# Kernel optimization log

Measured on AMD Instinct MI355X. Metric: run time of the kernel, lower is better.

The kernel has to match this reference:

```python
import jax, jax.numpy as jnp
import numpy as np

ALPHA = 0.2
NEG_INF = -9e15


def setup_inputs() -> dict:
    key = jax.random.key(0)
    k1, k2, k3, k4 = jax.random.split(key, 4)
    B, N, C_IN, C_OUT, R, H = 8, 1024, 256, 256, 4, 4
    node_feats = jax.random.normal(k1, (B, N, C_IN), dtype=jnp.float32)
    adj_matrix = jax.random.randint(k2, (B, N, N, R), 0, 2, dtype=jnp.int32)
    # xavier_uniform with gain=1.414 for Linear(c_in, c_out) weights
    lim_w = 1.414 * np.sqrt(6.0 / (C_IN + C_OUT))
    W = jax.random.uniform(k3, (R, C_IN, C_OUT), minval=-lim_w, maxval=lim_w, dtype=jnp.float32)
    c_per = C_OUT // H
    lim_a = 1.414 * np.sqrt(6.0 / (H + 2 * c_per))
    a = jax.random.uniform(k4, (R, H, 2 * c_per), minval=-lim_a, maxval=lim_a, dtype=jnp.float32)
    return {"node_feats": node_feats, "adj_matrix": adj_matrix, "W": W, "a": a}


def reference(node_feats, adj_matrix, W, a):
    B, N, _ = node_feats.shape
    R, H = a.shape[0], a.shape[1]
    C = a.shape[2] // 2  # per-head feature dim
    out = jnp.zeros((B, N, H, C), dtype=node_feats.dtype)
    for r in range(R):
        # per-relation projection: [B,N,H,C]
        f = jnp.einsum('bnc,cd->bnd', node_feats, W[r]).reshape(B, N, H, C)
        a_l, a_r = a[r, :, :C], a[r, :, C:]
        # attention logit decomposes: a . [f_i || f_j] = a_l . f_i + a_r . f_j
        li = jnp.einsum('bnhc,hc->bnh', f, a_l)  # source-node term
        lj = jnp.einsum('bnhc,hc->bnh', f, a_r)  # target-node term
        logits = jax.nn.leaky_relu(li[:, :, None, :] + lj[:, None, :, :], ALPHA)  # [B,N,N,H]
        mask = adj_matrix[..., r] != 0  # [B,N,N]
        logits = jnp.where(mask[..., None], logits, NEG_INF)
        probs = jax.nn.softmax(logits, axis=2)
        out = out + jnp.einsum('bijh,bjhc->bihc', probs, f)
    # concat_heads=True
    return out.reshape(B, N, H * C)
```

## Files before the change

### kernel.cpp

```cpp
#include <hip/hip_runtime.h>
#include <math.h>

#define Bsz 8
#define Nn 1024
#define CIN 256
#define COUT 256
#define NR 4
#define NH 4

typedef unsigned short u16;
typedef __attribute__((ext_vector_type(8))) short bf16x8;
typedef __attribute__((ext_vector_type(4))) float f32x4;
typedef __attribute__((ext_vector_type(2))) float f32x2;

#define OFF_EEI (16u << 20)
#define OFF_EEJ (17u << 20)
#define OFF_ADJM (18u << 20)
#define OFF_XBF (22u << 20)
#define OFF_WBFT (26u << 20)
#define OFF_WAL ((26u << 20) + (512u << 10))
#define OFF_WAR ((26u << 20) + (528u << 10))

#define LOG2E 1.4426950408889634f

__device__ __forceinline__ short f2bf(float x) {
  union { float f; unsigned u; } v; v.f = x;
  unsigned r = (v.u + 0x7FFFu + ((v.u >> 16) & 1u)) >> 16;
  return (short)r;
}

__device__ __forceinline__ float fast_exp2(float x) {
#if __has_builtin(__builtin_amdgcn_exp2f)
  return __builtin_amdgcn_exp2f(x);
#else
  return exp2f(x);
#endif
}

__device__ __forceinline__ int sbfe1(unsigned v, int bit) {
#if __has_builtin(__builtin_amdgcn_sbfe)
  return __builtin_amdgcn_sbfe((int)v, bit, 1);
#else
  return ((int)(v << (31 - bit))) >> 31;
#endif
}

__device__ __forceinline__ unsigned perm_hi16(unsigned hi, unsigned lo) {
#if __has_builtin(__builtin_amdgcn_perm)
  return __builtin_amdgcn_perm(hi, lo, 0x07060302u);
#else
  return (lo >> 16) | (hi & 0xFFFF0000u);
#endif
}

__device__ __forceinline__ void gl_lds16(const void* g, void* l) {
  __builtin_amdgcn_global_load_lds(
      (const __attribute__((address_space(1))) unsigned int*)(unsigned long long)g,
      (__attribute__((address_space(3))) unsigned int*)(unsigned int)(unsigned long long)l,
      16, 0, 0);
}

__global__ __launch_bounds__(256, 8)
void gatt_pack(const int4* __restrict__ adj4, unsigned long long* __restrict__ adjm) {
  const int t = threadIdx.x;
  const int wid = blockIdx.x * 4 + (t >> 6);
  const int lane = t & 63;
  const int jw = wid & 15;
  const int i = (wid >> 4) & 1023;
  const int b = wid >> 14;
  const int j = jw * 64 + lane;
  const int4 av = adj4[(size_t)(b * Nn + i) * Nn + j];
  const unsigned long long b0 = __ballot(av.x != 0);
  const unsigned long long b1 = __ballot(av.y != 0);
  const unsigned long long b2 = __ballot(av.z != 0);
  const unsigned long long b3 = __ballot(av.w != 0);
  if (lane < 4) {
    unsigned long long v = (lane == 0) ? b0 : (lane == 1) ? b1 : (lane == 2) ? b2 : b3;
    adjm[((size_t)((b * Nn + i) * NR + lane)) * 16 + jw] = v;
  }
}

__global__ __launch_bounds__(256, 4)
void gatt_prep(const float* __restrict__ W, const float* __restrict__ a,
               u16* __restrict__ WbfT, float* __restrict__ wa_l,
               float* __restrict__ wa_r) {
  const int t = threadIdx.x;
  if (blockIdx.x < 32) {
    const int r = blockIdx.x >> 3, kc = blockIdx.x & 7;
    u16 pk[32];
#pragma unroll 8
    for (int kk = 0; kk < 32; ++kk)
      pk[kk] = (u16)f2bf(W[(size_t)r * 65536 + (size_t)(kc * 32 + kk) * COUT + t]);
    u16* dst = WbfT + (size_t)r * 65536 + (size_t)t * CIN + kc * 32;
#pragma unroll
    for (int q = 0; q < 4; ++q) *(int4*)(dst + q * 8) = *(int4*)(pk + q * 8);
  } else {
    const int cb = blockIdx.x - 32;
    const int r = cb >> 2, h = cb & 3;
    float sl = 0.f, sr = 0.f;
    const float* Wp = W + (size_t)r * 65536 + (size_t)t * COUT + h * 64;
    const float* ap = a + r * 512 + h * 128;
#pragma unroll 8
    for (int c = 0; c < 64; ++c) {
      const float wv = Wp[c];
      sl = fmaf(wv, ap[c], sl);
      sr = fmaf(wv, ap[64 + c], sr);
    }
    wa_l[(size_t)cb * CIN + t] = sl;
    wa_r[(size_t)cb * CIN + t] = sr;
  }
}

__global__ __launch_bounds__(256, 4)
void gatt_logitx(const float* __restrict__ X, const float4* __restrict__ wal4,
                 const float4* __restrict__ war4, float2* __restrict__ EEi,
                 float2* __restrict__ EEj, u16* __restrict__ Xbf) {
  __shared__ float Xs[16 * 260];
  const int t = threadIdx.x;
  const int row0 = blockIdx.x * 16;
  {
    const int il = t >> 4, kq = t & 15;
    const float4* xp = (const float4*)(X + (size_t)(row0 + il) * CIN + kq * 16);
    float4 v[4];
    u16 pk[16];
#pragma unroll
    for (int u = 0; u < 4; ++u) {
      v[u] = xp[u];
      pk[u * 4 + 0] = (u16)f2bf(v[u].x);
      pk[u * 4 + 1] = (u16)f2bf(v[u].y);
      pk[u * 4 + 2] = (u16)f2bf(v[u].z);
      pk[u * 4 + 3] = (u16)f2bf(v[u].w);
    }
    float4* dst = (float4*)(Xs + il * 260 + kq * 16);
#pragma unroll
    for (int u = 0; u < 4; ++u) dst[u] = v[u];
    u16* xb = Xbf + (size_t)(row0 + il) * CIN + kq * 16;
    *(int4*)xb = *(int4*)pk;
    *(int4*)(xb + 8) = *(int4*)(pk + 8);
  }
  __syncthreads();
  const int rl = t >> 4, combo = t & 15;
  float li = 0.f, lj = 0.f;
#pragma unroll 8
  for (int k4 = 0; k4 < 64; ++k4) {
    const float4 x4 = *(const float4*)(Xs + rl * 260 + k4 * 4);
    const float4 wl = wal4[combo * 64 + k4];
    const float4 wr = war4[combo * 64 + k4];
    li += x4.x * wl.x + x4.y * wl.y + x4.z * wl.z + x4.w * wl.w;
    lj += x4.x * wr.x + x4.y * wr.y + x4.z * wr.z + x4.w * wr.w;
  }
  const int g = row0 + rl, b = g >> 10, n = g & 1023;
  const size_t idx = ((size_t)(combo * Bsz + b)) * Nn + n;
  const float lis = li * LOG2E, ljs = lj * LOG2E;
  EEi[idx] = make_float2(fast_exp2(lis), fast_exp2(0.2f * lis));
  EEj[idx] = make_float2(fast_exp2(ljs), fast_exp2(0.2f * ljs));
}

__global__ __launch_bounds__(256)
void gatt_fgemm(const u16* __restrict__ Xbf, const u16* __restrict__ WbfT,
                u16* __restrict__ fTf) {
  __shared__ u16 lds_w[8192];
  __shared__ u16 lds_x[2048];
  const int t = threadIdx.x;
  const int r = blockIdx.x & 3, b = (blockIdx.x >> 2) & 7, ntl = blockIdx.x >> 5;
  const int n0 = ntl * 64;
  const int g0 = b * Nn + n0;
  const int lane = t & 63, w = t >> 6;
  const int m = lane & 15, quad = lane >> 4;
  const int cw = w * 64;
  const int xq = quad ^ (m & 3);

  const u16* Wsrc = WbfT + (size_t)r * 65536;
  f32x4 acc[4][4];
#pragma unroll
  for (int ct = 0; ct < 4; ++ct)
#pragma unroll
    for (int nt = 0; nt < 4; ++nt) acc[ct][nt] = (f32x4){0.f, 0.f, 0.f, 0.f};

  for (int kc = 0; kc < 8; ++kc) {
    __syncthreads();
#pragma unroll
    for (int q = 0; q < 4; ++q) {
      const int s = q * 256 + t;
      const int c = s >> 2, ks = (s & 3) ^ (c & 3);
      gl_lds16(Wsrc + (size_t)c * CIN + kc * 32 + ks * 8, lds_w + s * 8);
    }
    {
      const int s = t;
      const int n = s >> 2, ks = (s & 3) ^ (n & 3);
      gl_lds16(Xbf + (size_t)(g0 + n) * CIN + kc * 32 + ks * 8, lds_x + s * 8);
    }
    __syncthreads();

    bf16x8 af[4], bfr[4];
#pragma unroll
    for (int ct = 0; ct < 4; ++ct)
      af[ct] = *(const bf16x8*)(lds_w + (cw + ct * 16 + m) * 32 + xq * 8);
#pragma unroll
    for (int nt = 0; nt < 4; ++nt)
      bfr[nt] = *(const bf16x8*)(lds_x + (nt * 16 + m) * 32 + xq * 8);
#pragma unroll
    for (int ct = 0; ct < 4; ++ct)
#pragma unroll
      for (int nt = 0; nt < 4; ++nt)
        acc[ct][nt] = __builtin_amdgcn_mfma_f32_16x16x32_bf16(af[ct], bfr[nt], acc[ct][nt], 0, 0, 0);
  }

  u16* fragbase = fTf + (size_t)(((r * Bsz + b) * 4 + w) * 128) * 512;
#pragma unroll
  for (int ct = 0; ct < 4; ++ct) {
#pragma unroll
    for (int ntf = 0; ntf < 4; ++ntf) {
      const int j = n0 + ntf * 16 + m;
      const int jb = j >> 5;
      const int qt = ((ntf & 1) << 1) | (m >> 3);
      const int e = m & 7;
      u16* dst = fragbase + (size_t)((jb * 4 + ct) * 512) + (qt * 16 + quad * 4) * 8 + e;
#pragma unroll
      for (int p = 0; p < 4; ++p) dst[p * 8] = (u16)f2bf(acc[ct][ntf][p]);
    }
  }
}

__global__ __launch_bounds__(1024, 4)
void gatt_attn(const unsigned long long* __restrict__ adjm,
               const u16* __restrict__ fTf, const float2* __restrict__ EEi,
               const float2* __restrict__ EEj, float* __restrict__ out) {
  __shared__ float smem[16384];

  const int t = threadIdx.x;
  const int b = blockIdx.x & 7;
  const int i0 = (blockIdx.x >> 3) * 32;
  const int w = t >> 6, lane = t & 63;
  const int r = w & 3, h = w >> 2;
  const int m = lane & 15, quad = lane >> 4;
  const int qo = quad * 8;
  const int combo = r * NH + h;

  const float2* EEib = EEi + ((size_t)(combo * Bsz + b)) * Nn;
  const float2 Li0 = EEib[i0 + m];
  const float2 Li1 = EEib[i0 + 16 + m];
  const f32x2 EI0 = {Li0.x, Li0.y};
  const f32x2 EI1 = {Li1.x, Li1.y};
  const float4* ej4 = (const float4*)(smem + combo * 1024);

  const unsigned long long* amp0 = adjm + ((size_t)((b * Nn + i0 + m) * NR + r)) * 16;
  const unsigned long long* amp1 = adjm + ((size_t)((b * Nn + i0 + 16 + m) * NR + r)) * 16;
  const bf16x8* fp = (const bf16x8*)fTf + (size_t)(((r * Bsz + b) * 4 + h)) * 8192;

  bf16x8 ones;
#pragma unroll
  for (int e = 0; e < 8; ++e) ones[e] = (short)0x3F80;

  f32x4 acc[2][4], den[2];
#pragma unroll
  for (int iw = 0; iw < 2; ++iw) {
    den[iw] = (f32x4){0.f, 0.f, 0.f, 0.f};
#pragma unroll
    for (int nt = 0; nt < 4; ++nt) acc[iw][nt] = (f32x4){0.f, 0.f, 0.f, 0.f};
  }

  for (int hs = 0; hs < 2; ++hs) {
    {
#pragma unroll
      for (int q = 0; q < 4; ++q) {
        const int s = q * 1024 + t;
        const int cb = s >> 8, off = s & 255;
        ((float4*)smem)[s] =
            ((const float4*)(EEj + ((size_t)(cb * Bsz + b)) * Nn))[hs * 256 + off];
      }
    }
    __syncthreads();

    for (int jq = hs * 8; jq < hs * 8 + 8; ++jq) {
      const uint2 mw0 = *(const uint2*)(amp0 + jq);
      const uint2 mw1 = *(const uint2*)(amp1 + jq);
#pragma unroll
      for (int half = 0; half < 2; ++half) {
        const int jb = jq * 2 + half;
        const int jbl = jb & 15;
        const unsigned mb0 = (half ? mw0.y : mw0.x) >> qo;
        const unsigned mb1 = (half ? mw1.y : mw1.x) >> qo;
        bf16x8 bfr[4];
#pragma unroll
        for (int nt = 0; nt < 4; ++nt) bfr[nt] = fp[(jb * 4 + nt) * 64 + lane];
        unsigned afu0[4], afu1[4];
#pragma unroll
        for (int pr = 0; pr < 4; ++pr) {
          const float4 v = ej4[jbl * 16 + quad * 4 + pr];
          const f32x2 v01 = {v.x, v.y};
          const f32x2 v23 = {v.z, v.w};
          {
            const f32x2 a0 = v01 * EI0;
            const f32x2 a1 = v23 * EI0;
            const unsigned e0 =
                __float_as_uint(fmaxf(a0.x, a0.y)) & (unsigned)sbfe1(mb0, 2 * pr);
            const unsigned e1 =
                __float_as_uint(fmaxf(a1.x, a1.y)) & (unsigned)sbfe1(mb0, 2 * pr + 1);
            afu0[pr] = perm_hi16(e1, e0);
          }
          {
            const f32x2 a0 = v01 * EI1;
            const f32x2 a1 = v23 * EI1;
            const unsigned e0 =
                __float_as_uint(fmaxf(a0.x, a0.y)) & (unsigned)sbfe1(mb1, 2 * pr);
            const unsigned e1 =
                __float_as_uint(fmaxf(a1.x, a1.y)) & (unsigned)sbfe1(mb1, 2 * pr + 1);
            afu1[pr] = perm_hi16(e1, e0);
          }
        }
        union { unsigned u[4]; bf16x8 v; } af0, af1;
#pragma unroll
        for (int pr = 0; pr < 4; ++pr) { af0.u[pr] = afu0[pr]; af1.u[pr] = afu1[pr]; }
        den[0] = __builtin_amdgcn_mfma_f32_16x16x32_bf16(af0.v, ones, den[0], 0, 0, 0);
#pragma unroll
        for (int nt = 0; nt < 4; ++nt)
          acc[0][nt] = __builtin_amdgcn_mfma_f32_16x16x32_bf16(af0.v, bfr[nt], acc[0][nt], 0, 0, 0);
        den[1] = __builtin_amdgcn_mfma_f32_16x16x32_bf16(af1.v, ones, den[1], 0, 0, 0);
#pragma unroll
        for (int nt = 0; nt < 4; ++nt)
          acc[1][nt] = __builtin_amdgcn_mfma_f32_16x16x32_bf16(af1.v, bfr[nt], acc[1][nt], 0, 0, 0);
      }
    }
    __syncthreads();
  }

#define OSTRIDE 260
#pragma unroll
  for (int rr = 0; rr < 4; ++rr) {
    if (r == rr) {
#pragma unroll
      for (int iw = 0; iw < 2; ++iw) {
#pragma unroll
        for (int p = 0; p < 4; ++p) {
          const float inv = __builtin_amdgcn_rcpf(den[iw][p]);
          float* op = smem + (iw * 16 + quad * 4 + p) * OSTRIDE + h * 64 + m;
#pragma unroll
          for (int nt = 0; nt < 4; ++nt) {
            const float v = acc[iw][nt][p] * inv;
            if (rr == 0) op[nt * 16] = v;
            else op[nt * 16] += v;
          }
        }
      }
    }
    __syncthreads();
  }

#pragma unroll
  for (int q = 0; q < 2; ++q) {
    const int idx = q * 1024 + t;
    const int row = idx >> 6, c4 = idx & 63;
    const float4 v = *(const float4*)(smem + row * OSTRIDE + c4 * 4);
    ((float4*)out)[((size_t)(b * Nn + i0 + row)) * 64 + c4] = v;
  }
}

extern "C" void kernel_launch(void* const* d_in, const int* in_sizes, int n_in,
                              void* d_out, int out_size, void* d_ws, size_t ws_size,
                              hipStream_t stream) {
  const float* X = (const float*)d_in[0];
  const int4* adj4 = (const int4*)d_in[1];
  const float* W = (const float*)d_in[2];
  const float* a = (const float*)d_in[3];
  float* out = (float*)d_out;

  char* ws = (char*)d_ws;
  u16* fTf = (u16*)ws;
  float2* EEi = (float2*)(ws + OFF_EEI);
  float2* EEj = (float2*)(ws + OFF_EEJ);
  unsigned long long* adjm = (unsigned long long*)(ws + OFF_ADJM);
  u16* Xbf = (u16*)(ws + OFF_XBF);
  u16* WbfT = (u16*)(ws + OFF_WBFT);
  float* wa_l = (float*)(ws + OFF_WAL);
  float* wa_r = (float*)(ws + OFF_WAR);

  gatt_pack<<<dim3(32768), dim3(256), 0, stream>>>(adj4, adjm);
  gatt_prep<<<dim3(48), dim3(256), 0, stream>>>(W, a, WbfT, wa_l, wa_r);
  gatt_logitx<<<dim3(512), dim3(256), 0, stream>>>(X, (const float4*)wa_l,
                                                   (const float4*)wa_r, EEi, EEj, Xbf);
  gatt_fgemm<<<dim3(512), dim3(256), 0, stream>>>(Xbf, WbfT, fTf);
  gatt_attn<<<dim3(256), dim3(1024), 0, stream>>>(adjm, fTf, EEi, EEj, out);
}
```

Baseline: 289.1 us.

## Split adjacency packing across prep, logit and GEMM kernels as extra blocks

Removes the standalone adjacency bit-packing kernel and spreads its 32768 blocks over the three preparatory kernels as extra trailing blocks. The bandwidth-bound packing can then run alongside the small, latency-bound prep, logit and projection GEMM work, which removes one launch and fills idle CUs. The risk is that the heavy packing blocks compete with the GEMM for bandwidth and occupancy. The GEMM kernel's launch bounds also limit how many packing blocks fit per CU.

```diff
diff --git a/kernel.cpp b/kernel.cpp
--- a/kernel.cpp
+++ b/kernel.cpp
@@ -23,6 +23,10 @@
 
 #define LOG2E 1.4426950408889634f
 
+#define PK_PREP 3072
+#define PK_LGX 6144
+#define PK_TOTAL 32768
+
 __device__ __forceinline__ short f2bf(float x) {
   union { float f; unsigned u; } v; v.f = x;
   unsigned r = (v.u + 0x7FFFu + ((v.u >> 16) & 1u)) >> 16;
@@ -60,10 +64,9 @@
       16, 0, 0);
 }
 
-__global__ __launch_bounds__(256, 8)
-void gatt_pack(const int4* __restrict__ adj4, unsigned long long* __restrict__ adjm) {
-  const int t = threadIdx.x;
-  const int wid = blockIdx.x * 4 + (t >> 6);
+__device__ __forceinline__ void pack_body(int pbid, int t, const int4* __restrict__ adj4,
+                                          unsigned long long* __restrict__ adjm) {
+  const int wid = pbid * 4 + (t >> 6);
   const int lane = t & 63;
   const int jw = wid & 15;
   const int i = (wid >> 4) & 1023;
@@ -83,8 +86,13 @@
 __global__ __launch_bounds__(256, 4)
 void gatt_prep(const float* __restrict__ W, const float* __restrict__ a,
                u16* __restrict__ WbfT, float* __restrict__ wa_l,
-               float* __restrict__ wa_r) {
+               float* __restrict__ wa_r, const int4* __restrict__ adj4,
+               unsigned long long* __restrict__ adjm) {
   const int t = threadIdx.x;
+  if (blockIdx.x >= 48) {
+    pack_body(blockIdx.x - 48, t, adj4, adjm);
+    return;
+  }
   if (blockIdx.x < 32) {
     const int r = blockIdx.x >> 3, kc = blockIdx.x & 7;
     u16 pk[32];
@@ -114,9 +122,14 @@
 __global__ __launch_bounds__(256, 4)
 void gatt_logitx(const float* __restrict__ X, const float4* __restrict__ wal4,
                  const float4* __restrict__ war4, float2* __restrict__ EEi,
-                 float2* __restrict__ EEj, u16* __restrict__ Xbf) {
+                 float2* __restrict__ EEj, u16* __restrict__ Xbf,
+                 const int4* __restrict__ adj4, unsigned long long* __restrict__ adjm) {
   __shared__ float Xs[16 * 260];
   const int t = threadIdx.x;
+  if (blockIdx.x >= 512) {
+    pack_body(blockIdx.x - 512 + PK_PREP, t, adj4, adjm);
+    return;
+  }
   const int row0 = blockIdx.x * 16;
   {
     const int il = t >> 4, kq = t & 15;
@@ -158,10 +171,15 @@
 
 __global__ __launch_bounds__(256)
 void gatt_fgemm(const u16* __restrict__ Xbf, const u16* __restrict__ WbfT,
-                u16* __restrict__ fTf) {
+                u16* __restrict__ fTf, const int4* __restrict__ adj4,
+                unsigned long long* __restrict__ adjm) {
   __shared__ u16 lds_w[8192];
   __shared__ u16 lds_x[2048];
   const int t = threadIdx.x;
+  if (blockIdx.x >= 512) {
+    pack_body(blockIdx.x - 512 + PK_PREP + PK_LGX, t, adj4, adjm);
+    return;
+  }
   const int r = blockIdx.x & 3, b = (blockIdx.x >> 2) & 7, ntl = blockIdx.x >> 5;
   const int n0 = ntl * 64;
   const int g0 = b * Nn + n0;
@@ -375,10 +393,11 @@
   float* wa_l = (float*)(ws + OFF_WAL);
   float* wa_r = (float*)(ws + OFF_WAR);
 
-  gatt_pack<<<dim3(32768), dim3(256), 0, stream>>>(adj4, adjm);
-  gatt_prep<<<dim3(48), dim3(256), 0, stream>>>(W, a, WbfT, wa_l, wa_r);
-  gatt_logitx<<<dim3(512), dim3(256), 0, stream>>>(X, (const float4*)wa_l,
-                                                   (const float4*)wa_r, EEi, EEj, Xbf);
-  gatt_fgemm<<<dim3(512), dim3(256), 0, stream>>>(Xbf, WbfT, fTf);
+  gatt_prep<<<dim3(48 + PK_PREP), dim3(256), 0, stream>>>(W, a, WbfT, wa_l, wa_r,
+                                                          adj4, adjm);
+  gatt_logitx<<<dim3(512 + PK_LGX), dim3(256), 0, stream>>>(
+      X, (const float4*)wa_l, (const float4*)wa_r, EEi, EEj, Xbf, adj4, adjm);
+  gatt_fgemm<<<dim3(512 + (PK_TOTAL - PK_PREP - PK_LGX)), dim3(256), 0, stream>>>(
+      Xbf, WbfT, fTf, adj4, adjm);
   gatt_attn<<<dim3(256), dim3(1024), 0, stream>>>(adjm, fTf, EEi, EEj, out);
 }
```

After: 283.2 us, median of 2. 1.02x faster.

## Fuse adjacency bit-packing into attention kernel with register-prefetched mask tiles

Applied to the files above, without the earlier changes.

Removes the separate adjacency pack kernel. The attention kernel now reads the int32 adjacency directly, ballots it into bitmasks held in shared memory, and prefetches the next 128-column chunk (adjacency and EEj) into registers while the MFMA work on the current chunk runs. This drops one kernel launch and the write and re-read of the packed mask through global memory. In exchange the attention kernel carries more registers and two barriers per chunk, and its 128 MB adjacency stream now overlaps with compute.

```diff
diff --git a/kernel.cpp b/kernel.cpp
--- a/kernel.cpp
+++ b/kernel.cpp
@@ -15,7 +15,6 @@
 
 #define OFF_EEI (16u << 20)
 #define OFF_EEJ (17u << 20)
-#define OFF_ADJM (18u << 20)
 #define OFF_XBF (22u << 20)
 #define OFF_WBFT (26u << 20)
 #define OFF_WAL ((26u << 20) + (512u << 10))
@@ -58,26 +57,6 @@
       (const __attribute__((address_space(1))) unsigned int*)(unsigned long long)g,
       (__attribute__((address_space(3))) unsigned int*)(unsigned int)(unsigned long long)l,
       16, 0, 0);
-}
-
-__global__ __launch_bounds__(256, 8)
-void gatt_pack(const int4* __restrict__ adj4, unsigned long long* __restrict__ adjm) {
-  const int t = threadIdx.x;
-  const int wid = blockIdx.x * 4 + (t >> 6);
-  const int lane = t & 63;
-  const int jw = wid & 15;
-  const int i = (wid >> 4) & 1023;
-  const int b = wid >> 14;
-  const int j = jw * 64 + lane;
-  const int4 av = adj4[(size_t)(b * Nn + i) * Nn + j];
-  const unsigned long long b0 = __ballot(av.x != 0);
-  const unsigned long long b1 = __ballot(av.y != 0);
-  const unsigned long long b2 = __ballot(av.z != 0);
-  const unsigned long long b3 = __ballot(av.w != 0);
-  if (lane < 4) {
-    unsigned long long v = (lane == 0) ? b0 : (lane == 1) ? b1 : (lane == 2) ? b2 : b3;
-    adjm[((size_t)((b * Nn + i) * NR + lane)) * 16 + jw] = v;
-  }
 }
 
 __global__ __launch_bounds__(256, 4)
@@ -223,10 +202,11 @@
 }
 
 __global__ __launch_bounds__(1024, 4)
-void gatt_attn(const unsigned long long* __restrict__ adjm,
-               const u16* __restrict__ fTf, const float2* __restrict__ EEi,
-               const float2* __restrict__ EEj, float* __restrict__ out) {
-  __shared__ float smem[16384];
+void gatt_attn(const int4* __restrict__ adj4, const u16* __restrict__ fTf,
+               const float2* __restrict__ EEi, const float2* __restrict__ EEj,
+               float* __restrict__ out) {
+  __shared__ float smem[8448];
+  unsigned long long* maskl = (unsigned long long*)(smem + 4096);
 
   const int t = threadIdx.x;
   const int b = blockIdx.x & 7;
@@ -242,11 +222,11 @@
   const float2 Li1 = EEib[i0 + 16 + m];
   const f32x2 EI0 = {Li0.x, Li0.y};
   const f32x2 EI1 = {Li1.x, Li1.y};
-  const float4* ej4 = (const float4*)(smem + combo * 1024);
-
-  const unsigned long long* amp0 = adjm + ((size_t)((b * Nn + i0 + m) * NR + r)) * 16;
-  const unsigned long long* amp1 = adjm + ((size_t)((b * Nn + i0 + 16 + m) * NR + r)) * 16;
-  const bf16x8* fp = (const bf16x8*)fTf + (size_t)(((r * Bsz + b) * 4 + h)) * 8192;
+
+  const bf16x8* fp = (const bf16x8*)fTf + (size_t)((r * Bsz + b) * 4 + h) * 8192;
+  const float4* ej4 = (const float4*)smem + combo * 64;
+  const float4* EEjw = (const float4*)(EEj + ((size_t)(w * Bsz + b)) * Nn);
+  const size_t arow = (size_t)(b * Nn + i0);
 
   bf16x8 ones;
 #pragma unroll
@@ -260,25 +240,54 @@
     for (int nt = 0; nt < 4; ++nt) acc[iw][nt] = (f32x4){0.f, 0.f, 0.f, 0.f};
   }
 
-  for (int hs = 0; hs < 2; ++hs) {
-    {
-#pragma unroll
-      for (int q = 0; q < 4; ++q) {
-        const int s = q * 1024 + t;
-        const int cb = s >> 8, off = s & 255;
-        ((float4*)smem)[s] =
-            ((const float4*)(EEj + ((size_t)(cb * Bsz + b)) * Nn))[hs * 256 + off];
-      }
-    }
-    __syncthreads();
-
-    for (int jq = hs * 8; jq < hs * 8 + 8; ++jq) {
-      const uint2 mw0 = *(const uint2*)(amp0 + jq);
-      const uint2 mw1 = *(const uint2*)(amp1 + jq);
+  int4 avv[4];
+  float4 ejv;
+
+#pragma unroll
+  for (int u = 0; u < 4; ++u) {
+    const int gu = w * 4 + u;
+    avv[u] = adj4[(arow + (gu >> 1)) * Nn + (gu & 1) * 64 + lane];
+  }
+  ejv = EEjw[lane];
+  {
+    unsigned long long my = 0;
+#pragma unroll
+    for (int u = 0; u < 4; ++u) {
+      const unsigned long long b0 = __ballot(avv[u].x != 0);
+      const unsigned long long b1 = __ballot(avv[u].y != 0);
+      const unsigned long long b2 = __ballot(avv[u].z != 0);
+      const unsigned long long b3 = __ballot(avv[u].w != 0);
+      if ((lane >> 4) == u) {
+        const int rr = (lane >> 2) & 3;
+        my = rr == 0 ? b0 : rr == 1 ? b1 : rr == 2 ? b2 : b3;
+      }
+    }
+    ((float4*)smem)[t] = ejv;
+    if ((lane & 3) == 0) {
+      const int gu = w * 4 + (lane >> 4);
+      maskl[(gu >> 1) * 9 + ((lane >> 2) & 3) * 2 + (gu & 1)] = my;
+    }
+  }
+  __syncthreads();
+
+  for (int p = 0; p < 8; ++p) {
+    if (p < 7) {
+#pragma unroll
+      for (int u = 0; u < 4; ++u) {
+        const int gu = w * 4 + u;
+        avv[u] = adj4[(arow + (gu >> 1)) * Nn + (p + 1) * 128 + (gu & 1) * 64 + lane];
+      }
+      ejv = EEjw[(p + 1) * 64 + lane];
+    }
+
+#pragma unroll
+    for (int jql = 0; jql < 2; ++jql) {
+      const uint2 mw0 = *(const uint2*)&maskl[m * 9 + r * 2 + jql];
+      const uint2 mw1 = *(const uint2*)&maskl[(16 + m) * 9 + r * 2 + jql];
 #pragma unroll
       for (int half = 0; half < 2; ++half) {
-        const int jb = jq * 2 + half;
-        const int jbl = jb & 15;
+        const int jb = p * 4 + jql * 2 + half;
+        const int jbl = jql * 2 + half;
         const unsigned mb0 = (half ? mw0.y : mw0.x) >> qo;
         const unsigned mb1 = (half ? mw1.y : mw1.x) >> qo;
         bf16x8 bfr[4];
@@ -322,6 +331,29 @@
           acc[1][nt] = __builtin_amdgcn_mfma_f32_16x16x32_bf16(af1.v, bfr[nt], acc[1][nt], 0, 0, 0);
       }
     }
+
+    unsigned long long my = 0;
+    if (p < 7) {
+#pragma unroll
+      for (int u = 0; u < 4; ++u) {
+        const unsigned long long b0 = __ballot(avv[u].x != 0);
+        const unsigned long long b1 = __ballot(avv[u].y != 0);
+        const unsigned long long b2 = __ballot(avv[u].z != 0);
+        const unsigned long long b3 = __ballot(avv[u].w != 0);
+        if ((lane >> 4) == u) {
+          const int rr = (lane >> 2) & 3;
+          my = rr == 0 ? b0 : rr == 1 ? b1 : rr == 2 ? b2 : b3;
+        }
+      }
+    }
+    __syncthreads();
+    if (p < 7) {
+      ((float4*)smem)[t] = ejv;
+      if ((lane & 3) == 0) {
+        const int gu = w * 4 + (lane >> 4);
+        maskl[(gu >> 1) * 9 + ((lane >> 2) & 3) * 2 + (gu & 1)] = my;
+      }
+    }
     __syncthreads();
   }
 
@@ -369,16 +401,14 @@
   u16* fTf = (u16*)ws;
   float2* EEi = (float2*)(ws + OFF_EEI);
   float2* EEj = (float2*)(ws + OFF_EEJ);
-  unsigned long long* adjm = (unsigned long long*)(ws + OFF_ADJM);
   u16* Xbf = (u16*)(ws + OFF_XBF);
   u16* WbfT = (u16*)(ws + OFF_WBFT);
   float* wa_l = (float*)(ws + OFF_WAL);
   float* wa_r = (float*)(ws + OFF_WAR);
 
-  gatt_pack<<<dim3(32768), dim3(256), 0, stream>>>(adj4, adjm);
   gatt_prep<<<dim3(48), dim3(256), 0, stream>>>(W, a, WbfT, wa_l, wa_r);
   gatt_logitx<<<dim3(512), dim3(256), 0, stream>>>(X, (const float4*)wa_l,
                                                    (const float4*)wa_r, EEi, EEj, Xbf);
   gatt_fgemm<<<dim3(512), dim3(256), 0, stream>>>(Xbf, WbfT, fTf);
-  gatt_attn<<<dim3(256), dim3(1024), 0, stream>>>(adjm, fTf, EEi, EEj, out);
-}
+  gatt_attn<<<dim3(256), dim3(1024), 0, stream>>>(adj4, fTf, EEi, EEj, out);
+}
```

Result: no change. 288.7 us (-0.1%).
